# Optimization experiments

Measured on AMD Instinct MI355X. Metric: run time of the kernel, lower is better.

## Reference

```python
import jax, jax.numpy as jnp
import numpy as np

D_MODEL = 1024
N_HEADS = 16
D_K = D_MODEL // N_HEADS
NEG = -1e10


def setup_inputs() -> dict:
    key = jax.random.key(0)
    ks = jax.random.split(key, 12)
    bs, sl = 2, 2048
    q = jax.random.normal(ks[0], (bs, sl, D_MODEL), dtype=jnp.float32)
    k = jax.random.normal(ks[1], (bs, sl, D_MODEL), dtype=jnp.float32)
    v = jax.random.normal(ks[2], (bs, sl, D_MODEL), dtype=jnp.float32)
    mask = jax.random.randint(ks[3], (bs, 1, sl, sl), 0, 2).astype(bool)
    s = 1.0 / np.sqrt(D_MODEL)
    Wq = jax.random.uniform(ks[4], (D_MODEL, D_MODEL), jnp.float32, -s, s)
    bq = jax.random.uniform(ks[5], (D_MODEL,), jnp.float32, -s, s)
    Wk = jax.random.uniform(ks[6], (D_MODEL, D_MODEL), jnp.float32, -s, s)
    bk = jax.random.uniform(ks[7], (D_MODEL,), jnp.float32, -s, s)
    Wv = jax.random.uniform(ks[8], (D_MODEL, D_MODEL), jnp.float32, -s, s)
    bv = jax.random.uniform(ks[9], (D_MODEL,), jnp.float32, -s, s)
    Wo = jax.random.uniform(ks[10], (D_MODEL, D_MODEL), jnp.float32, -s, s)
    bo = jax.random.uniform(ks[11], (D_MODEL,), jnp.float32, -s, s)
    return {"q": q, "k": k, "v": v, "mask": mask,
            "Wq": Wq, "bq": bq, "Wk": Wk, "bk": bk,
            "Wv": Wv, "bv": bv, "Wo": Wo, "bo": bo}


def reference(q, k, v, mask, Wq, bq, Wk, bk, Wv, bv, Wo, bo):
    bs, sl, _ = q.shape
    sl2 = k.shape[1]
    # linear projections (torch Linear: x @ W.T + b), split into heads: [b, h, s, d_k]
    qh = (q @ Wq.T + bq).reshape(bs, sl, N_HEADS, D_K).transpose(0, 2, 1, 3)
    kh = (k @ Wk.T + bk).reshape(bs, sl2, N_HEADS, D_K).transpose(0, 2, 1, 3)
    vh = (v @ Wv.T + bv).reshape(bs, sl2, N_HEADS, D_K).transpose(0, 2, 1, 3)
    scores = jnp.einsum('bhqd,bhkd->bhqk', qh, kh) / jnp.sqrt(jnp.float32(D_K))
    scores = jnp.where(mask, NEG, scores)
    attn = jax.nn.softmax(scores, axis=-1)
    z = jnp.einsum('bhqk,bhkd->bhqd', attn, vh)  # [b, h, sl, d_k]
    z = z.transpose(0, 2, 1, 3).reshape(bs, sl, D_MODEL)
    return z @ Wo.T + bo
```

## Files before the change

### kernel.cpp

```cpp
#include <hip/hip_runtime.h>

typedef __attribute__((ext_vector_type(8))) short short8;
typedef __attribute__((ext_vector_type(4))) float f32x4;
typedef __attribute__((ext_vector_type(16))) float f32x16;
typedef __attribute__((ext_vector_type(4))) unsigned int u32x4;

#define MFMA16(a, b, c) __builtin_amdgcn_mfma_f32_16x16x32_bf16((a), (b), (c), 0, 0, 0)
#define MFMA32(a, b, c) __builtin_amdgcn_mfma_f32_32x32x16_bf16((a), (b), (c), 0, 0, 0)

#if __has_builtin(__builtin_amdgcn_exp2f)
#define EXP2(x) __builtin_amdgcn_exp2f(x)
#else
#define EXP2(x) __expf((x) * 0.6931471805599453f)
#endif

__device__ __forceinline__ unsigned short f2bf(float f) {
  unsigned int u = __float_as_uint(f);
  u += 0x7FFFu + ((u >> 16) & 1u);
  return (unsigned short)(u >> 16);
}

__device__ __forceinline__ unsigned int cvtpk(float lo, float hi) {
  unsigned int r;
  asm("v_cvt_pk_bf16_f32 %0, %1, %2" : "=v"(r) : "v"(lo), "v"(hi));
  return r;
}

__device__ __forceinline__ float fmax3(float a, float b, float c) {
  return fmaxf(fmaxf(a, b), c);
}

__device__ __forceinline__ short8 mk8(unsigned int a, unsigned int b,
                                      unsigned int c, unsigned int d) {
  u32x4 u = {a, b, c, d};
  return __builtin_bit_cast(short8, u);
}

__device__ __forceinline__ void gload16(const void* g, void* l) {
  __builtin_amdgcn_global_load_lds((const __attribute__((address_space(1))) void*)g,
                                   (__attribute__((address_space(3))) void*)l, 16, 0, 0);
}

__device__ __forceinline__ short8 fragld64(const unsigned short* base, int row, int kchunk) {
  int cc = kchunk ^ (row & 7);
  return *(const short8*)(base + row * 64 + cc * 8);
}

__global__ void cvt3(const float* __restrict__ a, const float* __restrict__ b,
                     const float* __restrict__ c, unsigned short* __restrict__ out, int n4) {
  const float* src = (blockIdx.z == 0) ? a : ((blockIdx.z == 1) ? b : c);
  int i = blockIdx.x * blockDim.x + threadIdx.x;
  if (i >= n4) return;
  float4 v = ((const float4*)src)[i];
  ushort4 o;
  o.x = f2bf(v.x); o.y = f2bf(v.y); o.z = f2bf(v.z); o.w = f2bf(v.w);
  ((ushort4*)(out + (size_t)blockIdx.z * (size_t)n4 * 4))[i] = o;
}

__global__ void cvt4(const float* __restrict__ a, const float* __restrict__ b,
                     const float* __restrict__ c, const float* __restrict__ d,
                     unsigned short* __restrict__ out, int n4) {
  const float* src = (blockIdx.z == 0) ? a : ((blockIdx.z == 1) ? b
                   : ((blockIdx.z == 2) ? c : d));
  int i = blockIdx.x * blockDim.x + threadIdx.x;
  if (i >= n4) return;
  float4 v = ((const float4*)src)[i];
  ushort4 o;
  o.x = f2bf(v.x); o.y = f2bf(v.y); o.z = f2bf(v.z); o.w = f2bf(v.w);
  ((ushort4*)(out + (size_t)blockIdx.z * (size_t)n4 * 4))[i] = o;
}

__global__ void maskpack(const int* __restrict__ m, unsigned long long* __restrict__ mw) {
  const int lane = threadIdx.x & 63;
  const size_t wbase = ((size_t)blockIdx.x * (blockDim.x >> 6) + (threadIdx.x >> 6)) * 4ull;
#pragma unroll
  for (int u = 0; u < 4; ++u) {
    size_t word = wbase + u;
    int x = m[word * 64 + lane];
    unsigned long long bb = __ballot(x != 0);
    if (lane == 0) mw[word] = bb;
  }
}

__global__ void vtrans(const unsigned short* __restrict__ vh, unsigned short* __restrict__ vtg) {
  __shared__ unsigned short t[64][66];
  const int sx = blockIdx.x * 64, h = blockIdx.y, b = blockIdx.z;
  const int tid = threadIdx.x;
  const int r = tid >> 2, c0 = (tid & 3) * 16;
  const unsigned short* src = vh + ((size_t)(b * 2048 + sx + r)) * 1024 + h * 64 + c0;
  short8 x0 = *(const short8*)src;
  short8 x1 = *(const short8*)(src + 8);
#pragma unroll
  for (int e = 0; e < 8; ++e) {
    t[c0 + e][r] = (unsigned short)x0[e];
    t[c0 + 8 + e][r] = (unsigned short)x1[e];
  }
  __syncthreads();
  short8 y0, y1;
#pragma unroll
  for (int e = 0; e < 8; ++e) {
    y0[e] = (short)t[r][c0 + e];
    y1[e] = (short)t[r][c0 + 8 + e];
  }
  unsigned short* dst = vtg + ((size_t)((b * 16 + h) * 64 + r)) * 2048 + sx + c0;
  *(short8*)dst = y0;
  *(short8*)(dst + 8) = y1;
}

template<bool OUT_BF16>
__global__ __launch_bounds__(256, 3) void gemm_bt(
    const unsigned short* __restrict__ Abase, const unsigned short* __restrict__ Bbase,
    const float* __restrict__ bias0, const float* __restrict__ bias1,
    const float* __restrict__ bias2, void* __restrict__ outv, float scale0)
{
  constexpr int K = 1024, N = 1024;
  const int z = blockIdx.z;
  const unsigned short* A = Abase + (size_t)z * 4194304ull;
  const unsigned short* B = Bbase + (size_t)z * 1048576ull;
  const float* bias = (z == 0) ? bias0 : ((z == 1) ? bias1 : bias2);
  const float scale = (z == 0) ? scale0 : 1.0f;

  __shared__ unsigned short ldsA[128 * 64];
  __shared__ unsigned short ldsB[128 * 64];

  const int tid = threadIdx.x;
  const int lane = tid & 63, wid = tid >> 6;
  const int c16 = lane & 15, g = lane >> 4;
  const int m0 = blockIdx.y * 128, n0 = blockIdx.x * 128;
  const int wr = (wid >> 1) * 64, wc = (wid & 1) * 64;

  f32x4 acc[4][4] = {};

  for (int kt = 0; kt < K; kt += 64) {
    __syncthreads();
#pragma unroll
    for (int i = 0; i < 4; ++i) {
      int row = i * 32 + (tid >> 3);
      int cc = tid & 7;
      int scc = cc ^ (row & 7);
      gload16(A + (size_t)(m0 + row) * K + kt + scc * 8, ldsA + row * 64 + cc * 8);
      gload16(B + (size_t)(n0 + row) * K + kt + scc * 8, ldsB + row * 64 + cc * 8);
    }
    __syncthreads();
#pragma unroll
    for (int kc = 0; kc < 2; ++kc) {
      short8 af[4], bf[4];
#pragma unroll
      for (int mi = 0; mi < 4; ++mi) af[mi] = fragld64(ldsA, wr + mi * 16 + c16, kc * 4 + g);
#pragma unroll
      for (int ni = 0; ni < 4; ++ni) bf[ni] = fragld64(ldsB, wc + ni * 16 + c16, kc * 4 + g);
#pragma unroll
      for (int mi = 0; mi < 4; ++mi)
#pragma unroll
        for (int ni = 0; ni < 4; ++ni)
          acc[mi][ni] = MFMA16(af[mi], bf[ni], acc[mi][ni]);
    }
  }

#pragma unroll
  for (int mi = 0; mi < 4; ++mi)
#pragma unroll
    for (int ni = 0; ni < 4; ++ni) {
      int col = n0 + wc + ni * 16 + c16;
      float bb = bias[col];
#pragma unroll
      for (int r = 0; r < 4; ++r) {
        int row = m0 + wr + mi * 16 + g * 4 + r;
        float v = (acc[mi][ni][r] + bb) * scale;
        if constexpr (OUT_BF16)
          ((unsigned short*)outv)[(size_t)z * 4194304ull + (size_t)row * N + col] = f2bf(v);
        else
          ((float*)outv)[(size_t)row * N + col] = v;
      }
    }
}

__global__ __launch_bounds__(128, 2) void attn(
    const unsigned short* __restrict__ qh, const unsigned short* __restrict__ kh,
    const unsigned short* __restrict__ vtg, const unsigned long long* __restrict__ mw,
    unsigned short* __restrict__ zout)
{
  constexpr int SL = 2048, DM = 1024, NT = SL / 64;
  const int h = blockIdx.y, b = blockIdx.z;
  const int tid = threadIdx.x, lane = tid & 63, w = tid >> 6;
  const int ql = lane & 31;
  const int hd = lane >> 5;
  const int qa = blockIdx.x * 64 + w * 32;

  __shared__ unsigned short kbuf[2][4096];
  __shared__ unsigned short vbuf[2][4096];

  short8 qf[4];
  {
    const size_t qrow = ((size_t)b * SL + qa + ql) * DM + (size_t)h * 64 + hd * 8;
#pragma unroll
    for (int kc = 0; kc < 4; ++kc)
      qf[kc] = *(const short8*)(qh + qrow + kc * 16);
  }

  f32x16 zacc0 = {}, zacc1 = {};
  float mrun = -INFINITY, lrun = 0.f;

  const size_t kbase = (size_t)b * SL * DM + (size_t)h * 64;
  const size_t vbase = (size_t)((b * 16 + h) * 64) * (size_t)SL;
  const unsigned long long* mwq = mw + ((size_t)b * SL + qa + ql) * (SL / 64);

  const int sr = tid >> 3, scc = tid & 7;

  unsigned long long mwc = mwq[0];

#pragma unroll
  for (int i = 0; i < 4; ++i) {
    int row = sr + 16 * i;
    int sc8 = (scc ^ (row & 7)) * 8;
    gload16(kh + kbase + (size_t)row * DM + sc8, kbuf[0] + row * 64 + scc * 8);
    gload16(vtg + vbase + (size_t)row * SL + sc8, vbuf[0] + row * 64 + scc * 8);
  }

  for (int t = 0; t < NT; ++t) {
    const int cur = t & 1, nxt = cur ^ 1;
    __syncthreads();

    const bool more = (t + 1 < NT);
    unsigned long long mwn = 0;
    if (more) {
      const size_t ko = kbase + (size_t)(t + 1) * 64 * DM;
      const size_t vo = vbase + (size_t)(t + 1) * 64;
#pragma unroll
      for (int i = 0; i < 4; ++i) {
        int row = sr + 16 * i;
        int sc8 = (scc ^ (row & 7)) * 8;
        gload16(kh + ko + (size_t)row * DM + sc8, kbuf[nxt] + row * 64 + scc * 8);
        gload16(vtg + vo + (size_t)row * SL + sc8, vbuf[nxt] + row * 64 + scc * 8);
      }
      mwn = mwq[t + 1];
    }

    unsigned int b0 = ((unsigned int)mwc) >> (hd * 4);
    unsigned int b1 = ((unsigned int)(mwc >> 32)) >> (hd * 4);
    f32x16 s0, s1;
#pragma unroll
    for (int m = 0; m < 4; ++m) {
      unsigned int n0 = (b0 >> (m * 8)) & 0xFu;
      unsigned int n1 = (b1 >> (m * 8)) & 0xFu;
#pragma unroll
      for (int c = 0; c < 4; ++c) {
        s0[m * 4 + c] = ((n0 >> c) & 1u) ? -1e10f : 0.0f;
        s1[m * 4 + c] = ((n1 >> c) & 1u) ? -1e10f : 0.0f;
      }
    }

    __builtin_amdgcn_s_setprio(1);
#pragma unroll
    for (int kc = 0; kc < 4; ++kc) {
      short8 kf0 = fragld64(kbuf[cur], ql, kc * 2 + hd);
      short8 kf1 = fragld64(kbuf[cur], 32 + ql, kc * 2 + hd);
      s0 = MFMA32(kf0, qf[kc], s0);
      s1 = MFMA32(kf1, qf[kc], s1);
    }
    __builtin_amdgcn_s_setprio(0);

    float mx;
    {
      float t0 = fmax3(s0[0], s0[1], s0[2]);
      float t1 = fmax3(s0[3], s0[4], s0[5]);
      float t2 = fmax3(s0[6], s0[7], s0[8]);
      float t3 = fmax3(s0[9], s0[10], s0[11]);
      float t4 = fmax3(s0[12], s0[13], s0[14]);
      float t5 = fmax3(s0[15], s1[0], s1[1]);
      float t6 = fmax3(s1[2], s1[3], s1[4]);
      float t7 = fmax3(s1[5], s1[6], s1[7]);
      float t8 = fmax3(s1[8], s1[9], s1[10]);
      float t9 = fmax3(s1[11], s1[12], s1[13]);
      float ta = fmaxf(s1[14], s1[15]);
      float u0 = fmax3(t0, t1, t2);
      float u1 = fmax3(t3, t4, t5);
      float u2 = fmax3(t6, t7, t8);
      float u3 = fmaxf(t9, ta);
      mx = fmaxf(fmax3(u0, u1, u2), u3);
    }
    mx = fmaxf(mx, __shfl_xor(mx, 32));

    const bool defer = (__all(mx <= mrun + 8.f) != 0);
    const float mnew = defer ? mrun : fmaxf(mrun, mx);

#pragma unroll
    for (int i = 0; i < 16; ++i) {
      s0[i] = EXP2(s0[i] - mnew);
      s1[i] = EXP2(s1[i] - mnew);
    }
    float rs;
    {
      float a0 = (s0[0] + s0[1]) + (s0[2] + s0[3]);
      float a1 = (s0[4] + s0[5]) + (s0[6] + s0[7]);
      float a2 = (s0[8] + s0[9]) + (s0[10] + s0[11]);
      float a3 = (s0[12] + s0[13]) + (s0[14] + s0[15]);
      float a4 = (s1[0] + s1[1]) + (s1[2] + s1[3]);
      float a5 = (s1[4] + s1[5]) + (s1[6] + s1[7]);
      float a6 = (s1[8] + s1[9]) + (s1[10] + s1[11]);
      float a7 = (s1[12] + s1[13]) + (s1[14] + s1[15]);
      rs = ((a0 + a1) + (a2 + a3)) + ((a4 + a5) + (a6 + a7));
    }
    rs += __shfl_xor(rs, 32);

    if (defer) {
      lrun += rs;
    } else {
      float alpha = EXP2(mrun - mnew);
      mrun = mnew;
      lrun = lrun * alpha + rs;
#pragma unroll
      for (int reg = 0; reg < 16; ++reg) {
        float ar = __shfl(alpha, (reg & 3) + 8 * (reg >> 2) + 4 * hd);
        zacc0[reg] *= ar;
        zacc1[reg] *= ar;
      }
    }

    unsigned int wv[16];
#pragma unroll
    for (int i = 0; i < 8; ++i) wv[i] = cvtpk(s0[2 * i], s0[2 * i + 1]);
#pragma unroll
    for (int i = 0; i < 8; ++i) wv[8 + i] = cvtpk(s1[2 * i], s1[2 * i + 1]);
#pragma unroll
    for (int m = 0; m < 4; ++m) {
      asm("v_permlane32_swap_b32 %0, %1" : "+v"(wv[4 * m]), "+v"(wv[4 * m + 2]));
      asm("v_permlane32_swap_b32 %0, %1" : "+v"(wv[4 * m + 1]), "+v"(wv[4 * m + 3]));
    }

    __builtin_amdgcn_s_setprio(1);
#pragma unroll
    for (int m = 0; m < 4; ++m) {
      short8 pf = mk8(wv[4 * m], wv[4 * m + 1], wv[4 * m + 2], wv[4 * m + 3]);
      short8 vf0 = fragld64(vbuf[cur], ql, m * 2 + hd);
      short8 vf1 = fragld64(vbuf[cur], 32 + ql, m * 2 + hd);
      zacc0 = MFMA32(pf, vf0, zacc0);
      zacc1 = MFMA32(pf, vf1, zacc1);
    }
    __builtin_amdgcn_s_setprio(0);

    mwc = mwn;
  }

  float invl = 1.f / lrun;
#pragma unroll
  for (int reg = 0; reg < 16; ++reg) {
    int qrow = (reg & 3) + 8 * (reg >> 2) + 4 * hd;
    float il = __shfl(invl, qrow);
    size_t orow = ((size_t)b * SL + qa + qrow) * DM + (size_t)h * 64;
    zout[orow + ql] = f2bf(zacc0[reg] * il);
    zout[orow + 32 + ql] = f2bf(zacc1[reg] * il);
  }
}

extern "C" void kernel_launch(void* const* d_in, const int* in_sizes, int n_in,
                              void* d_out, int out_size, void* d_ws, size_t ws_size,
                              hipStream_t stream) {
  const float* q  = (const float*)d_in[0];
  const float* k  = (const float*)d_in[1];
  const float* v  = (const float*)d_in[2];
  const int* mask = (const int*)d_in[3];
  const float* Wq = (const float*)d_in[4];
  const float* bq = (const float*)d_in[5];
  const float* Wk = (const float*)d_in[6];
  const float* bk = (const float*)d_in[7];
  const float* Wv = (const float*)d_in[8];
  const float* bv = (const float*)d_in[9];
  const float* Wo = (const float*)d_in[10];
  const float* bo = (const float*)d_in[11];

  char* ws = (char*)d_ws;
  unsigned short* xbf = (unsigned short*)ws;
  unsigned long long* mwb = (unsigned long long*)ws;
  unsigned short* vtg = (unsigned short*)(ws + 2097152);
  unsigned short* wbf = (unsigned short*)(ws + 25165824);
  unsigned short* qkv = (unsigned short*)(ws + 33554432);
  unsigned short* zbf = (unsigned short*)(ws + 58720256);

  cvt3<<<dim3(4096, 1, 3), 256, 0, stream>>>(q, k, v, xbf, 1048576);
  cvt4<<<dim3(1024, 1, 4), 256, 0, stream>>>(Wq, Wk, Wv, Wo, wbf, 262144);

  gemm_bt<true><<<dim3(8, 32, 3), 256, 0, stream>>>(xbf, wbf, bq, bk, bv, (void*)qkv,
                                                    0.125f * 1.44269504088896f);
  maskpack<<<8192, 256, 0, stream>>>(mask, mwb);
  vtrans<<<dim3(32, 16, 2), 256, 0, stream>>>(qkv + 8388608ull, vtg);
  attn<<<dim3(32, 16, 2), 128, 0, stream>>>(qkv, qkv + 4194304ull, vtg, mwb, zbf);
  gemm_bt<false><<<dim3(8, 32, 1), 256, 0, stream>>>(zbf, wbf + 3145728ull, bo, bo, bo, d_out, 1.0f);
}
```

Measured before the change: 167.9 us.

## Split attention KV range in two and merge partial softmax results

Each attention block now handles only half of the key/value tiles, selected by a split index packed into a flattened 1D grid. This doubles the block count and halves per-block work. Each split writes a normalized partial output plus its running max and sum. A new combine kernel merges the two partials with log-sum-exp weights into the bf16 head-concatenated buffer. The goal is better CU load balance and shorter tails, in exchange for an extra kernel launch and extra global traffic for the partial outputs. The workspace is also re-laid out, with the V-transpose buffer now sharing space with the final z buffer.

```diff
diff --git a/kernel.cpp b/kernel.cpp
--- a/kernel.cpp
+++ b/kernel.cpp
@@ -18,6 +18,10 @@
   unsigned int u = __float_as_uint(f);
   u += 0x7FFFu + ((u >> 16) & 1u);
   return (unsigned short)(u >> 16);
+}
+
+__device__ __forceinline__ float bf2f(unsigned short u) {
+  return __uint_as_float(((unsigned int)u) << 16);
 }
 
 __device__ __forceinline__ unsigned int cvtpk(float lo, float hi) {
@@ -178,14 +182,20 @@
 __global__ __launch_bounds__(128, 2) void attn(
     const unsigned short* __restrict__ qh, const unsigned short* __restrict__ kh,
     const unsigned short* __restrict__ vtg, const unsigned long long* __restrict__ mw,
-    unsigned short* __restrict__ zout)
+    unsigned short* __restrict__ zn, float2* __restrict__ ml2)
 {
-  constexpr int SL = 2048, DM = 1024, NT = SL / 64;
-  const int h = blockIdx.y, b = blockIdx.z;
+  constexpr int SL = 2048, DM = 1024;
+  const int bid = blockIdx.x;
+  const int g = bid & 31;
+  const int u = bid >> 5;
+  const int s = u & 1;
+  const int qt = u >> 1;
+  const int h = g & 15, b = g >> 4;
+
   const int tid = threadIdx.x, lane = tid & 63, w = tid >> 6;
   const int ql = lane & 31;
   const int hd = lane >> 5;
-  const int qa = blockIdx.x * 64 + w * 32;
+  const int qa = qt * 64 + w * 32;
 
   __shared__ unsigned short kbuf[2][4096];
   __shared__ unsigned short vbuf[2][4096];
@@ -207,21 +217,22 @@
 
   const int sr = tid >> 3, scc = tid & 7;
 
-  unsigned long long mwc = mwq[0];
+  const int t0 = s * 16, t1 = t0 + 16;
+  unsigned long long mwc = mwq[t0];
 
 #pragma unroll
   for (int i = 0; i < 4; ++i) {
     int row = sr + 16 * i;
     int sc8 = (scc ^ (row & 7)) * 8;
-    gload16(kh + kbase + (size_t)row * DM + sc8, kbuf[0] + row * 64 + scc * 8);
-    gload16(vtg + vbase + (size_t)row * SL + sc8, vbuf[0] + row * 64 + scc * 8);
-  }
-
-  for (int t = 0; t < NT; ++t) {
+    gload16(kh + kbase + (size_t)(t0 * 64 + row) * DM + sc8, kbuf[0] + row * 64 + scc * 8);
+    gload16(vtg + vbase + (size_t)row * SL + t0 * 64 + sc8, vbuf[0] + row * 64 + scc * 8);
+  }
+
+  for (int t = t0; t < t1; ++t) {
     const int cur = t & 1, nxt = cur ^ 1;
     __syncthreads();
 
-    const bool more = (t + 1 < NT);
+    const bool more = (t + 1 < t1);
     unsigned long long mwn = 0;
     if (more) {
       const size_t ko = kbase + (size_t)(t + 1) * 64 * DM;
@@ -262,21 +273,21 @@
 
     float mx;
     {
-      float t0 = fmax3(s0[0], s0[1], s0[2]);
-      float t1 = fmax3(s0[3], s0[4], s0[5]);
-      float t2 = fmax3(s0[6], s0[7], s0[8]);
-      float t3 = fmax3(s0[9], s0[10], s0[11]);
-      float t4 = fmax3(s0[12], s0[13], s0[14]);
-      float t5 = fmax3(s0[15], s1[0], s1[1]);
-      float t6 = fmax3(s1[2], s1[3], s1[4]);
-      float t7 = fmax3(s1[5], s1[6], s1[7]);
-      float t8 = fmax3(s1[8], s1[9], s1[10]);
-      float t9 = fmax3(s1[11], s1[12], s1[13]);
-      float ta = fmaxf(s1[14], s1[15]);
-      float u0 = fmax3(t0, t1, t2);
-      float u1 = fmax3(t3, t4, t5);
-      float u2 = fmax3(t6, t7, t8);
-      float u3 = fmaxf(t9, ta);
+      float t0_ = fmax3(s0[0], s0[1], s0[2]);
+      float t1_ = fmax3(s0[3], s0[4], s0[5]);
+      float t2_ = fmax3(s0[6], s0[7], s0[8]);
+      float t3_ = fmax3(s0[9], s0[10], s0[11]);
+      float t4_ = fmax3(s0[12], s0[13], s0[14]);
+      float t5_ = fmax3(s0[15], s1[0], s1[1]);
+      float t6_ = fmax3(s1[2], s1[3], s1[4]);
+      float t7_ = fmax3(s1[5], s1[6], s1[7]);
+      float t8_ = fmax3(s1[8], s1[9], s1[10]);
+      float t9_ = fmax3(s1[11], s1[12], s1[13]);
+      float ta_ = fmaxf(s1[14], s1[15]);
+      float u0 = fmax3(t0_, t1_, t2_);
+      float u1 = fmax3(t3_, t4_, t5_);
+      float u2 = fmax3(t6_, t7_, t8_);
+      float u3 = fmaxf(t9_, ta_);
       mx = fmaxf(fmax3(u0, u1, u2), u3);
     }
     mx = fmaxf(mx, __shfl_xor(mx, 32));
@@ -342,15 +353,41 @@
     mwc = mwn;
   }
 
+  const int pbase = (g * 32 + qt) * 64 + w * 32;
   float invl = 1.f / lrun;
+  if (hd == 0) ml2[(size_t)(pbase + ql) * 2 + s] = make_float2(mrun, lrun);
 #pragma unroll
   for (int reg = 0; reg < 16; ++reg) {
     int qrow = (reg & 3) + 8 * (reg >> 2) + 4 * hd;
     float il = __shfl(invl, qrow);
-    size_t orow = ((size_t)b * SL + qa + qrow) * DM + (size_t)h * 64;
-    zout[orow + ql] = f2bf(zacc0[reg] * il);
-    zout[orow + 32 + ql] = f2bf(zacc1[reg] * il);
-  }
+    size_t zr = ((size_t)(pbase + qrow) * 2 + s) * 64;
+    zn[zr + ql] = f2bf(zacc0[reg] * il);
+    zn[zr + 32 + ql] = f2bf(zacc1[reg] * il);
+  }
+}
+
+__global__ void combine(const unsigned short* __restrict__ zn, const float2* __restrict__ ml2,
+                        unsigned short* __restrict__ zbf) {
+  int idx = blockIdx.x * 256 + threadIdx.x;
+  int p = idx >> 3, oct = idx & 7;
+  float2 a = ml2[(size_t)p * 2 + 0];
+  float2 c = ml2[(size_t)p * 2 + 1];
+  float m = fmaxf(a.x, c.x);
+  float w1 = (a.y > 0.f) ? a.y * EXP2(a.x - m) : 0.f;
+  float w2 = (c.y > 0.f) ? c.y * EXP2(c.x - m) : 0.f;
+  float tot = w1 + w2;
+  float inv = (tot > 0.f) ? 1.f / tot : 0.f;
+  w1 *= inv; w2 *= inv;
+  short8 x1 = *(const short8*)(zn + ((size_t)p * 2 + 0) * 64 + oct * 8);
+  short8 x2 = *(const short8*)(zn + ((size_t)p * 2 + 1) * 64 + oct * 8);
+  int g = p >> 11, srow = p & 2047;
+  int h = g & 15, b = g >> 4;
+  unsigned short* dst = zbf + ((size_t)(b * 2048 + srow)) * 1024 + h * 64 + oct * 8;
+  short8 o;
+#pragma unroll
+  for (int e = 0; e < 8; ++e)
+    o[e] = (short)f2bf(w1 * bf2f((unsigned short)x1[e]) + w2 * bf2f((unsigned short)x2[e]));
+  *(short8*)dst = o;
 }
 
 extern "C" void kernel_launch(void* const* d_in, const int* in_sizes, int n_in,
@@ -372,9 +409,11 @@
   char* ws = (char*)d_ws;
   unsigned short* xbf = (unsigned short*)ws;
   unsigned long long* mwb = (unsigned long long*)ws;
-  unsigned short* vtg = (unsigned short*)(ws + 2097152);
+  unsigned short* zn  = (unsigned short*)(ws + 1048576);
+  float2* ml2         = (float2*)(ws + 17825792);
   unsigned short* wbf = (unsigned short*)(ws + 25165824);
   unsigned short* qkv = (unsigned short*)(ws + 33554432);
+  unsigned short* vtg = (unsigned short*)(ws + 58720256);
   unsigned short* zbf = (unsigned short*)(ws + 58720256);
 
   cvt3<<<dim3(4096, 1, 3), 256, 0, stream>>>(q, k, v, xbf, 1048576);
@@ -384,6 +423,7 @@
                                                     0.125f * 1.44269504088896f);
   maskpack<<<8192, 256, 0, stream>>>(mask, mwb);
   vtrans<<<dim3(32, 16, 2), 256, 0, stream>>>(qkv + 8388608ull, vtg);
-  attn<<<dim3(32, 16, 2), 128, 0, stream>>>(qkv, qkv + 4194304ull, vtg, mwb, zbf);
+  attn<<<2048, 128, 0, stream>>>(qkv, qkv + 4194304ull, vtg, mwb, zn, ml2);
+  combine<<<2048, 256, 0, stream>>>(zn, ml2, zbf);
   gemm_bt<false><<<dim3(8, 32, 1), 256, 0, stream>>>(zbf, wbf + 3145728ull, bo, bo, bo, d_out, 1.0f);
 }
```

Measured after the change: 174.1 us. 1.04x slower.
